# Performance work log

Measured on AMD Instinct MI355X. Metric: run time of the kernel, lower is better.

The kernel has to match this reference:

```python
import jax, jax.numpy as jnp
import numpy as np

B, N, E = 2, 5000, 160000
F_IN, HID, ED = 128, 128, 16
IN_EDGE = 2 * F_IN + 16 + ED  # source, target, radial(4*4), edge_attr


def _lin(k, fan_in, fan_out):
    return (jax.random.normal(k, (fan_in, fan_out), jnp.float32) / np.sqrt(fan_in)).astype(jnp.float32)


def setup_inputs() -> dict:
    key = jax.random.key(0)
    ks = jax.random.split(key, 16)
    h = jax.random.normal(ks[0], (B, N, F_IN), jnp.float32)
    coord = jax.random.normal(ks[1], (B, N, 4, 3), jnp.float32)
    edge_index = jax.random.randint(ks[2], (2, E), 0, N)
    edge_attr = jax.random.normal(ks[3], (E, ED), jnp.float32)
    return {
        "h": h, "coord": coord, "edge_index": edge_index, "edge_attr": edge_attr,
        # edge_mlp: Linear(IN_EDGE->HID), ReLU, Linear(HID->HID), ReLU
        "W_e1": _lin(ks[4], IN_EDGE, HID), "b_e1": jnp.zeros((HID,), jnp.float32),
        "W_e2": _lin(ks[5], HID, HID), "b_e2": jnp.zeros((HID,), jnp.float32),
        # node_mlp: Linear(HID+F_IN->HID), ReLU, Linear(HID->F_IN)
        "W_n1": _lin(ks[6], HID + F_IN, HID), "b_n1": jnp.zeros((HID,), jnp.float32),
        "W_n2": _lin(ks[7], HID, F_IN), "b_n2": jnp.zeros((F_IN,), jnp.float32),
        # coord_mlp: Linear(HID->HID), ReLU, Linear(HID->4, bias=False, xavier gain 0.001)
        "W_c1": _lin(ks[8], HID, HID), "b_c1": jnp.zeros((HID,), jnp.float32),
        "W_c2": _lin(ks[9], HID, 4) * 0.001,
    }


def reference(h, coord, edge_index, edge_attr,
              W_e1, b_e1, W_e2, b_e2,
              W_n1, b_n1, W_n2, b_n2,
              W_c1, b_c1, W_c2):
    row, col = edge_index[0], edge_index[1]
    coords_weight = 1.0
    n_nodes = h.shape[1]

    def single(h_b, coord_b):
        # coord2radial
        cd = coord_b[row] - coord_b[col]                                  # [E,4,3]
        prod = jnp.einsum('ejt,ekt->ejk', cd, cd).reshape(cd.shape[0], -1)  # [E,16]
        nrm = jnp.linalg.norm(prod, axis=-1, keepdims=True)
        radial = prod / jnp.maximum(nrm, 1e-12)                           # F.normalize
        # edge_model
        x = jnp.concatenate([h_b[row], h_b[col], radial, edge_attr], axis=-1)
        ef = jax.nn.relu(jax.nn.relu(x @ W_e1 + b_e1) @ W_e2 + b_e2)      # [E,HID]
        # coord_model: segment mean of cd * coord_mlp(ef)
        w = jax.nn.relu(ef @ W_c1 + b_c1) @ W_c2                          # [E,4]
        trans = cd * w[:, :, None]                                        # [E,4,3]
        agg_c = jax.ops.segment_sum(trans, row, num_segments=n_nodes)     # [N,4,3]
        cnt = jax.ops.segment_sum(jnp.ones((row.shape[0],), trans.dtype), row,
                                  num_segments=n_nodes)                   # [N]
        coord_new = coord_b + (agg_c / jnp.maximum(cnt, 1.0)[:, None, None]) * coords_weight
        # node_model (recurrent)
        agg_h = jax.ops.segment_sum(ef, row, num_segments=n_nodes)        # [N,HID]
        z = jnp.concatenate([h_b, agg_h], axis=-1)
        h_new = h_b + jax.nn.relu(z @ W_n1 + b_n1) @ W_n2 + b_n2
        return h_new, coord_new

    hs, coords = jax.vmap(single)(h, coord)
    return hs, coords
```

## Files before the change

kernel.cpp:

```cpp
#include <hip/hip_runtime.h>
#include <hip/hip_bf16.h>

#define B   2
#define NN_ 5000
#define NE_ 160000
#define F   128
#define HID 128
#define ED  16

typedef __bf16 bf16x8 __attribute__((ext_vector_type(8)));
typedef __bf16 bf16x4 __attribute__((ext_vector_type(4)));
typedef float  f32x4  __attribute__((ext_vector_type(4)));

#define MS  136
#define PS  40
#define EDG 128

__global__ void pack_weights(const float* __restrict__ We1, const float* __restrict__ We2,
                             const float* __restrict__ Wc1, const float* __restrict__ Wc2,
                             __bf16* __restrict__ pw1, __bf16* __restrict__ pw2,
                             __bf16* __restrict__ pwc1, __bf16* __restrict__ pwc2)
{
    int idx = blockIdx.x * 256 + threadIdx.x;
    const float* W; __bf16* P; int KT, Nr, local;
    if (idx < 36864)      { W = We1; P = pw1;  KT = 9; Nr = 128; local = idx; }
    else if (idx < 53248) { W = We2; P = pw2;  KT = 4; Nr = 128; local = idx - 36864; }
    else if (idx < 69632) { W = Wc1; P = pwc1; KT = 4; Nr = 128; local = idx - 53248; }
    else                  { W = Wc2; P = pwc2; KT = 4; Nr = 4;   local = idx - 69632; }
    int j = local & 7, lane = (local >> 3) & 63, rest = local >> 9;
    int kt = rest % KT, nt = rest / KT;
    int k = kt * 32 + (lane >> 4) * 8 + j;
    int n = nt * 16 + (lane & 15);
    float v = (n < Nr) ? W[k * Nr + n] : 0.f;
    P[local] = (__bf16)v;
}

__global__ void hist_kernel(const int* __restrict__ ei, int* __restrict__ csr_cnt)
{
    int i = blockIdx.x * 256 + threadIdx.x;
    if (i < NE_) atomicAdd(&csr_cnt[ei[i]], 1);
}

__global__ void scan_kernel(const int* __restrict__ csr_cnt,
                            int* __restrict__ csr_off, int* __restrict__ csr_pos)
{
    __shared__ int part[256];
    const int t = threadIdx.x;
    int sum = 0;
    #pragma unroll
    for (int j = 0; j < 20; j++) {
        int idx = t * 20 + j;
        if (idx < NN_) sum += csr_cnt[idx];
    }
    part[t] = sum;
    __syncthreads();
    if (t == 0) {
        int run = 0;
        for (int i = 0; i < 256; i++) { int v = part[i]; part[i] = run; run += v; }
    }
    __syncthreads();
    int run = part[t];
    #pragma unroll
    for (int j = 0; j < 20; j++) {
        int idx = t * 20 + j;
        if (idx < NN_) { csr_off[idx] = run; csr_pos[idx] = run; run += csr_cnt[idx]; }
    }
    if (t == 0) csr_off[NN_] = NE_;
}

__global__ void bucket_kernel(const int* __restrict__ ei,
                              int* __restrict__ csr_pos, int* __restrict__ bucket)
{
    int i = blockIdx.x * 256 + threadIdx.x;
    if (i < NE_) { int p = atomicAdd(&csr_pos[ei[i]], 1); bucket[p] = i; }
}

__global__ void ea_sort_kernel(const float* __restrict__ ea, const int* __restrict__ bucket,
                               __bf16* __restrict__ eas)
{
    int idx = blockIdx.x * 256 + threadIdx.x;
    if (idx < NE_ * 4) {
        int p = idx >> 2, j = idx & 3;
        int e = bucket[p];
        float4 v = ((const float4*)ea)[e * 4 + j];
        bf16x4 bv = {(__bf16)v.x, (__bf16)v.y, (__bf16)v.z, (__bf16)v.w};
        *(bf16x4*)&eas[p * 16 + j * 4] = bv;
    }
}

__global__ __launch_bounds__(512) void pre_kernel(
    const float* __restrict__ h, const __bf16* __restrict__ pw1,
    __bf16* __restrict__ pr, __bf16* __restrict__ pc)
{
    __shared__ __align__(16) __bf16 hs[128 * MS];
    const int t = threadIdx.x;
    const int b = blockIdx.y;
    const int n0 = blockIdx.x * 128;
    const int lane = t & 63, wave = t >> 6;
    const int quad = lane >> 4, c = lane & 15;

    #pragma unroll
    for (int it = 0; it < 8; it++) {
        int idx = it * 512 + t;
        int node = idx >> 5, ch = idx & 31;
        int gn = n0 + node;
        float4 v = (gn < NN_) ? *(const float4*)&h[((size_t)b * NN_ + gn) * F + ch * 4]
                              : (float4){0.f, 0.f, 0.f, 0.f};
        bf16x4 bv = {(__bf16)v.x, (__bf16)v.y, (__bf16)v.z, (__bf16)v.w};
        *(bf16x4*)&hs[node * MS + ch * 4] = bv;
    }
    __syncthreads();

    const bf16x8* pw1v = (const bf16x8*)pw1;
    f32x4 accr[8], accc[8];
    #pragma unroll
    for (int m = 0; m < 8; m++) { accr[m] = (f32x4){0,0,0,0}; accc[m] = (f32x4){0,0,0,0}; }
    for (int kt = 0; kt < 4; kt++) {
        bf16x8 wr = pw1v[(wave * 9 + kt) * 64 + lane];
        bf16x8 wc = pw1v[(wave * 9 + kt + 4) * 64 + lane];
        #pragma unroll
        for (int m = 0; m < 8; m++) {
            bf16x8 x = *(const bf16x8*)&hs[(m * 16 + c) * MS + kt * 32 + quad * 8];
            accr[m] = __builtin_amdgcn_mfma_f32_16x16x32_bf16(wr, x, accr[m], 0, 0, 0);
            accc[m] = __builtin_amdgcn_mfma_f32_16x16x32_bf16(wc, x, accc[m], 0, 0, 0);
        }
    }
    #pragma unroll
    for (int m = 0; m < 8; m++) {
        int gn = n0 + m * 16 + c;
        if (gn < NN_) {
            size_t base = ((size_t)b * NN_ + gn) * F + wave * 16 + quad * 4;
            bf16x4 orr = {(__bf16)accr[m][0], (__bf16)accr[m][1], (__bf16)accr[m][2], (__bf16)accr[m][3]};
            bf16x4 occ = {(__bf16)accc[m][0], (__bf16)accc[m][1], (__bf16)accc[m][2], (__bf16)accc[m][3]};
            *(bf16x4*)&pr[base] = orr;
            *(bf16x4*)&pc[base] = occ;
        }
    }
}

__global__ __launch_bounds__(512, 4) void edge_kernel(
    const __bf16* __restrict__ pr, const __bf16* __restrict__ pc,
    const float* __restrict__ coord,
    const int* __restrict__ ei, const __bf16* __restrict__ eas,
    const int* __restrict__ bucket,
    const float* __restrict__ be1, const float* __restrict__ be2,
    const float* __restrict__ bc1,
    const __bf16* __restrict__ pw1, const __bf16* __restrict__ pw2,
    const __bf16* __restrict__ pwc1, const __bf16* __restrict__ pwc2,
    float* __restrict__ agg_h, float* __restrict__ agg_c)
{
    __shared__ __align__(16) __bf16 buf1[EDG * MS];
    __shared__ __align__(16) __bf16 buf2[EDG * MS];
    __shared__ __bf16 cds[EDG][12];
    __shared__ int rs[EDG], cs[EDG];

    const int t = threadIdx.x;
    const int b = blockIdx.y;
    const int p0 = blockIdx.x * EDG;
    const int lane = t & 63, wave = t >> 6;
    const int quad = lane >> 4, c = lane & 15;
    const int mh = wave >> 2, np = wave & 3;

    if (t < EDG) {
        int eid = bucket[p0 + t];
        rs[t] = ei[eid]; cs[t] = ei[NE_ + eid];
    }
    __syncthreads();

    const __bf16* prb = pr + (size_t)b * NN_ * F;
    const __bf16* pcb = pc + (size_t)b * NN_ * F;
    #pragma unroll
    for (int it = 0; it < 4; it++) {
        int idx = it * 512 + t;
        int e = idx >> 4, ch = idx & 15;
        bf16x8 a = *(const bf16x8*)(prb + (size_t)rs[e] * F + ch * 8);
        bf16x8 v = *(const bf16x8*)(pcb + (size_t)cs[e] * F + ch * 8);
        bf16x8 o;
        #pragma unroll
        for (int j = 0; j < 8; j++) o[j] = (__bf16)((float)a[j] + (float)v[j]);
        *(bf16x8*)&buf1[e * MS + ch * 8] = o;
    }
    if (t < EDG) {
        int e = t;
        const float* cr = coord + ((size_t)b * NN_ + rs[e]) * 12;
        const float* cc = coord + ((size_t)b * NN_ + cs[e]) * 12;
        float cd[12];
        #pragma unroll
        for (int j = 0; j < 12; j++) { cd[j] = cr[j] - cc[j]; cds[e][j] = (__bf16)cd[j]; }
        float prod[16]; float ss = 0.f;
        #pragma unroll
        for (int j = 0; j < 4; j++)
            #pragma unroll
            for (int k = 0; k < 4; k++) {
                float p = cd[j*3]*cd[k*3] + cd[j*3+1]*cd[k*3+1] + cd[j*3+2]*cd[k*3+2];
                prod[j*4 + k] = p; ss += p * p;
            }
        float inv = 1.0f / fmaxf(sqrtf(ss), 1e-12f);
        #pragma unroll
        for (int j = 0; j < 16; j++) buf2[e * PS + j] = (__bf16)(prod[j] * inv);
        const uint4* ep = (const uint4*)(eas + (size_t)(p0 + e) * 16);
        *(uint4*)&buf2[e * PS + 16] = ep[0];
        *(uint4*)&buf2[e * PS + 24] = ep[1];
    }
    __syncthreads();

    const bf16x8* pw1v  = (const bf16x8*)pw1;
    const bf16x8* pw2v  = (const bf16x8*)pw2;
    const bf16x8* pwc1v = (const bf16x8*)pwc1;
    const bf16x8* pwc2v = (const bf16x8*)pwc2;

    f32x4 acc1[4][2];
    #pragma unroll
    for (int m = 0; m < 4; m++)
        #pragma unroll
        for (int n = 0; n < 2; n++) acc1[m][n] = (f32x4){0,0,0,0};
    {
        bf16x8 x1[4];
        #pragma unroll
        for (int m = 0; m < 4; m++)
            x1[m] = *(const bf16x8*)&buf2[((mh*4 + m)*16 + c) * PS + quad*8];
        #pragma unroll
        for (int n = 0; n < 2; n++) {
            bf16x8 w = pw1v[((2*np + n)*9 + 8)*64 + lane];
            #pragma unroll
            for (int m = 0; m < 4; m++)
                acc1[m][n] = __builtin_amdgcn_mfma_f32_16x16x32_bf16(w, x1[m], acc1[m][n], 0, 0, 0);
        }
    }
    #pragma unroll
    for (int n = 0; n < 2; n++) {
        int nt = 2*np + n;
        float4 bb = *(const float4*)&be1[nt*16 + quad*4];
        #pragma unroll
        for (int m = 0; m < 4; m++) {
            int row = (mh*4 + m)*16 + c;
            bf16x4 p = *(const bf16x4*)&buf1[row * MS + nt*16 + quad*4];
            bf16x4 o = { (__bf16)fmaxf(acc1[m][n][0] + (float)p[0] + bb.x, 0.f),
                         (__bf16)fmaxf(acc1[m][n][1] + (float)p[1] + bb.y, 0.f),
                         (__bf16)fmaxf(acc1[m][n][2] + (float)p[2] + bb.z, 0.f),
                         (__bf16)fmaxf(acc1[m][n][3] + (float)p[3] + bb.w, 0.f) };
            *(bf16x4*)&buf1[row * MS + nt*16 + quad*4] = o;
        }
    }
    __syncthreads();

    f32x4 acc2[4][2];
    #pragma unroll
    for (int m = 0; m < 4; m++)
        #pragma unroll
        for (int n = 0; n < 2; n++) acc2[m][n] = (f32x4){0,0,0,0};
    for (int kt = 0; kt < 4; kt++) {
        bf16x8 x[4];
        #pragma unroll
        for (int m = 0; m < 4; m++)
            x[m] = *(const bf16x8*)&buf1[((mh*4 + m)*16 + c) * MS + kt*32 + quad*8];
        #pragma unroll
        for (int n = 0; n < 2; n++) {
            bf16x8 w = pw2v[((2*np + n)*4 + kt)*64 + lane];
            #pragma unroll
            for (int m = 0; m < 4; m++)
                acc2[m][n] = __builtin_amdgcn_mfma_f32_16x16x32_bf16(w, x[m], acc2[m][n], 0, 0, 0);
        }
    }
    #pragma unroll
    for (int n = 0; n < 2; n++) {
        int nt = 2*np + n;
        float4 bb = *(const float4*)&be2[nt*16 + quad*4];
        #pragma unroll
        for (int m = 0; m < 4; m++) {
            int row = (mh*4 + m)*16 + c;
            bf16x4 o = { (__bf16)fmaxf(acc2[m][n][0] + bb.x, 0.f),
                         (__bf16)fmaxf(acc2[m][n][1] + bb.y, 0.f),
                         (__bf16)fmaxf(acc2[m][n][2] + bb.z, 0.f),
                         (__bf16)fmaxf(acc2[m][n][3] + bb.w, 0.f) };
            *(bf16x4*)&buf2[row * MS + nt*16 + quad*4] = o;
        }
    }
    __syncthreads();

    f32x4 acc3[4][2];
    #pragma unroll
    for (int m = 0; m < 4; m++)
        #pragma unroll
        for (int n = 0; n < 2; n++) acc3[m][n] = (f32x4){0,0,0,0};
    for (int kt = 0; kt < 4; kt++) {
        bf16x8 x[4];
        #pragma unroll
        for (int m = 0; m < 4; m++)
            x[m] = *(const bf16x8*)&buf2[((mh*4 + m)*16 + c) * MS + kt*32 + quad*8];
        #pragma unroll
        for (int n = 0; n < 2; n++) {
            bf16x8 w = pwc1v[((2*np + n)*4 + kt)*64 + lane];
            #pragma unroll
            for (int m = 0; m < 4; m++)
                acc3[m][n] = __builtin_amdgcn_mfma_f32_16x16x32_bf16(w, x[m], acc3[m][n], 0, 0, 0);
        }
    }
    #pragma unroll
    for (int n = 0; n < 2; n++) {
        int nt = 2*np + n;
        float4 bb = *(const float4*)&bc1[nt*16 + quad*4];
        #pragma unroll
        for (int m = 0; m < 4; m++) {
            int row = (mh*4 + m)*16 + c;
            bf16x4 o = { (__bf16)fmaxf(acc3[m][n][0] + bb.x, 0.f),
                         (__bf16)fmaxf(acc3[m][n][1] + bb.y, 0.f),
                         (__bf16)fmaxf(acc3[m][n][2] + bb.z, 0.f),
                         (__bf16)fmaxf(acc3[m][n][3] + bb.w, 0.f) };
            *(bf16x4*)&buf1[row * MS + nt*16 + quad*4] = o;
        }
    }
    __syncthreads();

    f32x4 accw = (f32x4){0,0,0,0};
    for (int kt = 0; kt < 4; kt++) {
        bf16x8 x = *(const bf16x8*)&buf1[(wave*16 + c) * MS + kt*32 + quad*8];
        accw = __builtin_amdgcn_mfma_f32_16x16x32_bf16(pwc2v[kt*64 + lane], x, accw, 0, 0, 0);
    }
    if (quad == 0) {
        int e = wave*16 + c;
        #pragma unroll
        for (int j = 0; j < 12; j++)
            cds[e][j] = (__bf16)((float)cds[e][j] * accw[j/3]);
    }
    __syncthreads();

    {
        float* aggh_b = agg_h + (size_t)b * NN_ * HID;
        const int col = t & 127, seg = t >> 7;
        float run = 0.f;
        int cur = rs[seg * 32];
        for (int e = seg * 32; e < seg * 32 + 32; e++) {
            int r = rs[e];
            float v = (float)buf2[e * MS + col];
            if (r != cur) {
                atomicAdd(&aggh_b[(size_t)cur * HID + col], run);
                run = 0.f; cur = r;
            }
            run += v;
        }
        atomicAdd(&aggh_b[(size_t)cur * HID + col], run);
    }
    if (t < 96) {
        float* aggc_b = agg_c + (size_t)b * NN_ * 12;
        const int j = t % 12, q = t / 12;
        float run = 0.f;
        int cur = rs[q * 16];
        for (int e = q * 16; e < q * 16 + 16; e++) {
            int r = rs[e];
            float v = (float)cds[e][j];
            if (r != cur) {
                atomicAdd(&aggc_b[(size_t)cur * 12 + j], run);
                run = 0.f; cur = r;
            }
            run += v;
        }
        atomicAdd(&aggc_b[(size_t)cur * 12 + j], run);
    }
}

#define NPB 8
__global__ __launch_bounds__(128) void node_kernel(
    const float* __restrict__ h, const float* __restrict__ agg_h,
    const float* __restrict__ Wn1, const float* __restrict__ bn1,
    const float* __restrict__ Wn2, const float* __restrict__ bn2,
    float* __restrict__ out_h)
{
    __shared__ float zs[NPB][2 * F];
    __shared__ float h1[NPB][HID];
    const int t  = threadIdx.x;
    const int b  = blockIdx.y;
    const int n0 = blockIdx.x * NPB;

    #pragma unroll
    for (int i = 0; i < NPB; i++) {
        size_t base = ((size_t)b * NN_ + n0 + i);
        zs[i][t]     = h[base * F + t];
        zs[i][F + t] = agg_h[base * HID + t];
    }
    __syncthreads();

    float acc[NPB];
    #pragma unroll
    for (int i = 0; i < NPB; i++) acc[i] = bn1[t];
    for (int k = 0; k < 2 * F; k += 4) {
        float w0 = Wn1[(k+0)*HID + t], w1 = Wn1[(k+1)*HID + t];
        float w2 = Wn1[(k+2)*HID + t], w3 = Wn1[(k+3)*HID + t];
        #pragma unroll
        for (int i = 0; i < NPB; i++) {
            float4 xv = *(const float4*)&zs[i][k];
            acc[i] += xv.x*w0 + xv.y*w1 + xv.z*w2 + xv.w*w3;
        }
    }
    __syncthreads();
    #pragma unroll
    for (int i = 0; i < NPB; i++) h1[i][t] = fmaxf(acc[i], 0.f);
    __syncthreads();

    #pragma unroll
    for (int i = 0; i < NPB; i++) acc[i] = bn2[t];
    for (int k = 0; k < HID; k += 4) {
        float w0 = Wn2[(k+0)*F + t], w1 = Wn2[(k+1)*F + t];
        float w2 = Wn2[(k+2)*F + t], w3 = Wn2[(k+3)*F + t];
        #pragma unroll
        for (int i = 0; i < NPB; i++) {
            float4 xv = *(const float4*)&h1[i][k];
            acc[i] += xv.x*w0 + xv.y*w1 + xv.z*w2 + xv.w*w3;
        }
    }
    #pragma unroll
    for (int i = 0; i < NPB; i++) {
        size_t base = ((size_t)b * NN_ + n0 + i);
        out_h[base * F + t] = zs[i][t] + acc[i];
    }
}

__global__ void coord_kernel(
    const float* __restrict__ coord, const float* __restrict__ agg_c,
    const int* __restrict__ csr_off, float* __restrict__ out_c)
{
    int i = blockIdx.x * 256 + threadIdx.x;
    if (i < B * NN_ * 12) {
        int node = i / 12;
        int n = node % NN_;
        float deg = (float)(csr_off[n + 1] - csr_off[n]);
        out_c[i] = coord[i] + agg_c[i] / fmaxf(deg, 1.0f);
    }
}

extern "C" void kernel_launch(void* const* d_in, const int* in_sizes, int n_in,
                              void* d_out, int out_size, void* d_ws, size_t ws_size,
                              hipStream_t stream) {
    const float* h     = (const float*)d_in[0];
    const float* coord = (const float*)d_in[1];
    const int*   ei    = (const int*)d_in[2];
    const float* ea    = (const float*)d_in[3];
    const float* We1   = (const float*)d_in[4];
    const float* be1   = (const float*)d_in[5];
    const float* We2   = (const float*)d_in[6];
    const float* be2   = (const float*)d_in[7];
    const float* Wn1   = (const float*)d_in[8];
    const float* bn1   = (const float*)d_in[9];
    const float* Wn2   = (const float*)d_in[10];
    const float* bn2   = (const float*)d_in[11];
    const float* Wc1   = (const float*)d_in[12];
    const float* bc1   = (const float*)d_in[13];
    const float* Wc2   = (const float*)d_in[14];

    float* out_h = (float*)d_out;
    float* out_c = out_h + (size_t)B * NN_ * F;

    unsigned char* base = (unsigned char*)d_ws;
    __bf16* pw1  = (__bf16*)base;
    __bf16* pw2  = pw1 + 36864;
    __bf16* pwc1 = pw2 + 16384;
    __bf16* pwc2 = pwc1 + 16384;
    unsigned char* dyn = base + 143360;

    int* csr_cnt = (int*)(dyn);
    int* csr_off = (int*)(dyn + 20000);
    int* csr_pos = (int*)(dyn + 40016);
    int* bucket  = (int*)(dyn + 60016);
    float* agg_h = (float*)(dyn + 700016);
    float* agg_c = agg_h + (size_t)B * NN_ * HID;
    __bf16* pr   = (__bf16*)(agg_c + (size_t)B * NN_ * 12);
    __bf16* pc   = pr + (size_t)B * NN_ * F;
    __bf16* eas  = pc + (size_t)B * NN_ * F;

    pack_weights<<<280, 256, 0, stream>>>(We1, We2, Wc1, Wc2, pw1, pw2, pwc1, pwc2);

    hipMemsetAsync(csr_cnt, 0, 20000, stream);
    hipMemsetAsync(agg_h, 0, (size_t)B * NN_ * (HID + 12) * sizeof(float), stream);

    hist_kernel<<<625, 256, 0, stream>>>(ei, csr_cnt);
    scan_kernel<<<1, 256, 0, stream>>>(csr_cnt, csr_off, csr_pos);
    bucket_kernel<<<625, 256, 0, stream>>>(ei, csr_pos, bucket);

    dim3 pg((NN_ + 127) / 128, B);
    pre_kernel<<<pg, 512, 0, stream>>>(h, pw1, pr, pc);

    ea_sort_kernel<<<2500, 256, 0, stream>>>(ea, bucket, eas);

    dim3 eg(NE_ / EDG, B);
    edge_kernel<<<eg, 512, 0, stream>>>(pr, pc, coord, ei, eas, bucket, be1, be2, bc1,
                                        pw1, pw2, pwc1, pwc2, agg_h, agg_c);

    dim3 ng(NN_ / NPB, B);
    node_kernel<<<ng, 128, 0, stream>>>(h, agg_h, Wn1, bn1, Wn2, bn2, out_h);

    int cn = (B * NN_ * 12 + 255) / 256;
    coord_kernel<<<cn, 256, 0, stream>>>(coord, agg_c, csr_off, out_c);
}
```

Measured before the change: 236.6 us.

## Move node MLP to bf16 MFMA, fuse coord update and edge-attr sorting

Rewrites the node MLP from scalar fp32 FMAs into bf16 MFMA tiles, 32 nodes per block, with Wn1/Wn2 prepacked by pack_weights. The coordinate update is folded into the node kernel and the edge-attribute sort into the bucket kernel, which removes two launches. This cuts per-node ALU work and launch overhead. In exchange the node MLP inputs and hidden activations are rounded to bf16, adding precision error.

New measurement: 208.5 us. 11.9% less time.

```diff
diff --git a/kernel.cpp b/kernel.cpp
--- a/kernel.cpp
+++ b/kernel.cpp
@@ -15,18 +15,25 @@
 #define MS  136
 #define PS  40
 #define EDG 128
+#define ZS  264
+#define HS  136
+#define NPB2 32
 
 __global__ void pack_weights(const float* __restrict__ We1, const float* __restrict__ We2,
                              const float* __restrict__ Wc1, const float* __restrict__ Wc2,
+                             const float* __restrict__ Wn1, const float* __restrict__ Wn2,
                              __bf16* __restrict__ pw1, __bf16* __restrict__ pw2,
-                             __bf16* __restrict__ pwc1, __bf16* __restrict__ pwc2)
+                             __bf16* __restrict__ pwc1, __bf16* __restrict__ pwc2,
+                             __bf16* __restrict__ pwn1, __bf16* __restrict__ pwn2)
 {
     int idx = blockIdx.x * 256 + threadIdx.x;
     const float* W; __bf16* P; int KT, Nr, local;
-    if (idx < 36864)      { W = We1; P = pw1;  KT = 9; Nr = 128; local = idx; }
-    else if (idx < 53248) { W = We2; P = pw2;  KT = 4; Nr = 128; local = idx - 36864; }
-    else if (idx < 69632) { W = Wc1; P = pwc1; KT = 4; Nr = 128; local = idx - 53248; }
-    else                  { W = Wc2; P = pwc2; KT = 4; Nr = 4;   local = idx - 69632; }
+    if (idx < 36864)       { W = We1; P = pw1;  KT = 9; Nr = 128; local = idx; }
+    else if (idx < 53248)  { W = We2; P = pw2;  KT = 4; Nr = 128; local = idx - 36864; }
+    else if (idx < 69632)  { W = Wc1; P = pwc1; KT = 4; Nr = 128; local = idx - 53248; }
+    else if (idx < 71680)  { W = Wc2; P = pwc2; KT = 4; Nr = 4;   local = idx - 69632; }
+    else if (idx < 104448) { W = Wn1; P = pwn1; KT = 8; Nr = 128; local = idx - 71680; }
+    else                   { W = Wn2; P = pwn2; KT = 4; Nr = 128; local = idx - 104448; }
     int j = local & 7, lane = (local >> 3) & 63, rest = local >> 9;
     int kt = rest % KT, nt = rest / KT;
     int k = kt * 32 + (lane >> 4) * 8 + j;
@@ -68,23 +75,22 @@
     if (t == 0) csr_off[NN_] = NE_;
 }
 
-__global__ void bucket_kernel(const int* __restrict__ ei,
-                              int* __restrict__ csr_pos, int* __restrict__ bucket)
+__global__ void bucket_kernel(const int* __restrict__ ei, const float* __restrict__ ea,
+                              int* __restrict__ csr_pos, int* __restrict__ bucket,
+                              __bf16* __restrict__ eas)
 {
     int i = blockIdx.x * 256 + threadIdx.x;
-    if (i < NE_) { int p = atomicAdd(&csr_pos[ei[i]], 1); bucket[p] = i; }
-}
-
-__global__ void ea_sort_kernel(const float* __restrict__ ea, const int* __restrict__ bucket,
-                               __bf16* __restrict__ eas)
-{
-    int idx = blockIdx.x * 256 + threadIdx.x;
-    if (idx < NE_ * 4) {
-        int p = idx >> 2, j = idx & 3;
-        int e = bucket[p];
-        float4 v = ((const float4*)ea)[e * 4 + j];
-        bf16x4 bv = {(__bf16)v.x, (__bf16)v.y, (__bf16)v.z, (__bf16)v.w};
-        *(bf16x4*)&eas[p * 16 + j * 4] = bv;
+    if (i < NE_) {
+        int p = atomicAdd(&csr_pos[ei[i]], 1);
+        bucket[p] = i;
+        const float4* src = (const float4*)(ea + (size_t)i * ED);
+        __bf16* dst = eas + (size_t)p * ED;
+        #pragma unroll
+        for (int j = 0; j < 4; j++) {
+            float4 v = src[j];
+            bf16x4 bv = {(__bf16)v.x, (__bf16)v.y, (__bf16)v.z, (__bf16)v.w};
+            *(bf16x4*)&dst[j * 4] = bv;
+        }
     }
 }
 
@@ -359,72 +365,127 @@
     }
 }
 
-#define NPB 8
-__global__ __launch_bounds__(128) void node_kernel(
+__global__ __launch_bounds__(256) void node_kernel(
     const float* __restrict__ h, const float* __restrict__ agg_h,
-    const float* __restrict__ Wn1, const float* __restrict__ bn1,
-    const float* __restrict__ Wn2, const float* __restrict__ bn2,
-    float* __restrict__ out_h)
-{
-    __shared__ float zs[NPB][2 * F];
-    __shared__ float h1[NPB][HID];
-    const int t  = threadIdx.x;
-    const int b  = blockIdx.y;
-    const int n0 = blockIdx.x * NPB;
-
-    #pragma unroll
-    for (int i = 0; i < NPB; i++) {
-        size_t base = ((size_t)b * NN_ + n0 + i);
-        zs[i][t]     = h[base * F + t];
-        zs[i][F + t] = agg_h[base * HID + t];
-    }
-    __syncthreads();
-
-    float acc[NPB];
-    #pragma unroll
-    for (int i = 0; i < NPB; i++) acc[i] = bn1[t];
-    for (int k = 0; k < 2 * F; k += 4) {
-        float w0 = Wn1[(k+0)*HID + t], w1 = Wn1[(k+1)*HID + t];
-        float w2 = Wn1[(k+2)*HID + t], w3 = Wn1[(k+3)*HID + t];
-        #pragma unroll
-        for (int i = 0; i < NPB; i++) {
-            float4 xv = *(const float4*)&zs[i][k];
-            acc[i] += xv.x*w0 + xv.y*w1 + xv.z*w2 + xv.w*w3;
-        }
-    }
-    __syncthreads();
-    #pragma unroll
-    for (int i = 0; i < NPB; i++) h1[i][t] = fmaxf(acc[i], 0.f);
-    __syncthreads();
-
-    #pragma unroll
-    for (int i = 0; i < NPB; i++) acc[i] = bn2[t];
-    for (int k = 0; k < HID; k += 4) {
-        float w0 = Wn2[(k+0)*F + t], w1 = Wn2[(k+1)*F + t];
-        float w2 = Wn2[(k+2)*F + t], w3 = Wn2[(k+3)*F + t];
-        #pragma unroll
-        for (int i = 0; i < NPB; i++) {
-            float4 xv = *(const float4*)&h1[i][k];
-            acc[i] += xv.x*w0 + xv.y*w1 + xv.z*w2 + xv.w*w3;
-        }
-    }
-    #pragma unroll
-    for (int i = 0; i < NPB; i++) {
-        size_t base = ((size_t)b * NN_ + n0 + i);
-        out_h[base * F + t] = zs[i][t] + acc[i];
-    }
-}
-
-__global__ void coord_kernel(
-    const float* __restrict__ coord, const float* __restrict__ agg_c,
-    const int* __restrict__ csr_off, float* __restrict__ out_c)
-{
-    int i = blockIdx.x * 256 + threadIdx.x;
-    if (i < B * NN_ * 12) {
-        int node = i / 12;
-        int n = node % NN_;
-        float deg = (float)(csr_off[n + 1] - csr_off[n]);
-        out_c[i] = coord[i] + agg_c[i] / fmaxf(deg, 1.0f);
+    const float* __restrict__ agg_c, const float* __restrict__ coord,
+    const int* __restrict__ csr_off,
+    const __bf16* __restrict__ pwn1, const float* __restrict__ bn1,
+    const __bf16* __restrict__ pwn2, const float* __restrict__ bn2,
+    float* __restrict__ out_h, float* __restrict__ out_c)
+{
+    __shared__ __align__(16) __bf16 zs[NPB2 * ZS];
+    __shared__ __align__(16) __bf16 h1s[NPB2 * HS];
+    const int t = threadIdx.x;
+    const int b = blockIdx.y;
+    const int n0 = blockIdx.x * NPB2;
+    const int lane = t & 63, wave = t >> 6;
+    const int quad = lane >> 4, c = lane & 15;
+
+    #pragma unroll
+    for (int it = 0; it < 8; it++) {
+        int idx = it * 256 + t;
+        int node = idx >> 6, ch = idx & 63;
+        int gn = n0 + node;
+        float4 v = (float4){0.f, 0.f, 0.f, 0.f};
+        if (gn < NN_) {
+            const float* src = (ch < 32) ? &h[((size_t)b * NN_ + gn) * F + ch * 4]
+                                         : &agg_h[((size_t)b * NN_ + gn) * HID + (ch - 32) * 4];
+            v = *(const float4*)src;
+        }
+        bf16x4 bv = {(__bf16)v.x, (__bf16)v.y, (__bf16)v.z, (__bf16)v.w};
+        *(bf16x4*)&zs[node * ZS + ch * 4] = bv;
+    }
+    __syncthreads();
+
+    const bf16x8* w1v = (const bf16x8*)pwn1;
+    const bf16x8* w2v = (const bf16x8*)pwn2;
+    f32x4 a1[2][2];
+    #pragma unroll
+    for (int m = 0; m < 2; m++)
+        #pragma unroll
+        for (int n = 0; n < 2; n++) a1[m][n] = (f32x4){0,0,0,0};
+    for (int kt = 0; kt < 8; kt++) {
+        bf16x8 x[2];
+        #pragma unroll
+        for (int m = 0; m < 2; m++)
+            x[m] = *(const bf16x8*)&zs[(m*16 + c) * ZS + kt*32 + quad*8];
+        #pragma unroll
+        for (int n = 0; n < 2; n++) {
+            bf16x8 w = w1v[((2*wave + n)*8 + kt)*64 + lane];
+            #pragma unroll
+            for (int m = 0; m < 2; m++)
+                a1[m][n] = __builtin_amdgcn_mfma_f32_16x16x32_bf16(w, x[m], a1[m][n], 0, 0, 0);
+        }
+    }
+    __syncthreads();
+    #pragma unroll
+    for (int n = 0; n < 2; n++) {
+        int nt = 2*wave + n;
+        float4 bb = *(const float4*)&bn1[nt*16 + quad*4];
+        #pragma unroll
+        for (int m = 0; m < 2; m++) {
+            bf16x4 o = { (__bf16)fmaxf(a1[m][n][0] + bb.x, 0.f),
+                         (__bf16)fmaxf(a1[m][n][1] + bb.y, 0.f),
+                         (__bf16)fmaxf(a1[m][n][2] + bb.z, 0.f),
+                         (__bf16)fmaxf(a1[m][n][3] + bb.w, 0.f) };
+            *(bf16x4*)&h1s[(m*16 + c) * HS + nt*16 + quad*4] = o;
+        }
+    }
+    __syncthreads();
+
+    f32x4 a2[2][2];
+    #pragma unroll
+    for (int m = 0; m < 2; m++)
+        #pragma unroll
+        for (int n = 0; n < 2; n++) a2[m][n] = (f32x4){0,0,0,0};
+    for (int kt = 0; kt < 4; kt++) {
+        bf16x8 x[2];
+        #pragma unroll
+        for (int m = 0; m < 2; m++)
+            x[m] = *(const bf16x8*)&h1s[(m*16 + c) * HS + kt*32 + quad*8];
+        #pragma unroll
+        for (int n = 0; n < 2; n++) {
+            bf16x8 w = w2v[((2*wave + n)*4 + kt)*64 + lane];
+            #pragma unroll
+            for (int m = 0; m < 2; m++)
+                a2[m][n] = __builtin_amdgcn_mfma_f32_16x16x32_bf16(w, x[m], a2[m][n], 0, 0, 0);
+        }
+    }
+    float* os = (float*)zs;
+    #pragma unroll
+    for (int n = 0; n < 2; n++) {
+        int nt = 2*wave + n;
+        float4 bb = *(const float4*)&bn2[nt*16 + quad*4];
+        #pragma unroll
+        for (int m = 0; m < 2; m++) {
+            f32x4 o = { a2[m][n][0] + bb.x, a2[m][n][1] + bb.y,
+                        a2[m][n][2] + bb.z, a2[m][n][3] + bb.w };
+            *(f32x4*)&os[(m*16 + c) * 132 + nt*16 + quad*4] = o;
+        }
+    }
+    __syncthreads();
+
+    #pragma unroll
+    for (int it = 0; it < 4; it++) {
+        int idx = it * 256 + t;
+        int node = idx >> 5, ch = idx & 31;
+        int gn = n0 + node;
+        if (gn < NN_) {
+            size_t gb = ((size_t)b * NN_ + gn) * F + ch * 4;
+            float4 hres = *(const float4*)&h[gb];
+            float4 acc = *(const float4*)&os[node * 132 + ch * 4];
+            float4 o = { hres.x + acc.x, hres.y + acc.y, hres.z + acc.z, hres.w + acc.w };
+            *(float4*)&out_h[gb] = o;
+        }
+    }
+    for (int idx = t; idx < NPB2 * 12; idx += 256) {
+        int node = idx / 12, j = idx % 12;
+        int gn = n0 + node;
+        if (gn < NN_) {
+            float deg = (float)(csr_off[gn + 1] - csr_off[gn]);
+            size_t ci = ((size_t)b * NN_ + gn) * 12 + j;
+            out_c[ci] = coord[ci] + agg_c[ci] / fmaxf(deg, 1.0f);
+        }
     }
 }
 
@@ -455,7 +516,9 @@
     __bf16* pw2  = pw1 + 36864;
     __bf16* pwc1 = pw2 + 16384;
     __bf16* pwc2 = pwc1 + 16384;
-    unsigned char* dyn = base + 143360;
+    __bf16* pwn1 = pwc2 + 2048;
+    __bf16* pwn2 = pwn1 + 32768;
+    unsigned char* dyn = base + 241664;
 
     int* csr_cnt = (int*)(dyn);
     int* csr_off = (int*)(dyn + 20000);
@@ -467,27 +530,24 @@
     __bf16* pc   = pr + (size_t)B * NN_ * F;
     __bf16* eas  = pc + (size_t)B * NN_ * F;
 
-    pack_weights<<<280, 256, 0, stream>>>(We1, We2, Wc1, Wc2, pw1, pw2, pwc1, pwc2);
+    pack_weights<<<472, 256, 0, stream>>>(We1, We2, Wc1, Wc2, Wn1, Wn2,
+                                          pw1, pw2, pwc1, pwc2, pwn1, pwn2);
 
     hipMemsetAsync(csr_cnt, 0, 20000, stream);
     hipMemsetAsync(agg_h, 0, (size_t)B * NN_ * (HID + 12) * sizeof(float), stream);
 
     hist_kernel<<<625, 256, 0, stream>>>(ei, csr_cnt);
     scan_kernel<<<1, 256, 0, stream>>>(csr_cnt, csr_off, csr_pos);
-    bucket_kernel<<<625, 256, 0, stream>>>(ei, csr_pos, bucket);
+    bucket_kernel<<<625, 256, 0, stream>>>(ei, ea, csr_pos, bucket, eas);
 
     dim3 pg((NN_ + 127) / 128, B);
     pre_kernel<<<pg, 512, 0, stream>>>(h, pw1, pr, pc);
-
-    ea_sort_kernel<<<2500, 256, 0, stream>>>(ea, bucket, eas);
 
     dim3 eg(NE_ / EDG, B);
     edge_kernel<<<eg, 512, 0, stream>>>(pr, pc, coord, ei, eas, bucket, be1, be2, bc1,
                                         pw1, pw2, pwc1, pwc2, agg_h, agg_c);
 
-    dim3 ng(NN_ / NPB, B);
-    node_kernel<<<ng, 128, 0, stream>>>(h, agg_h, Wn1, bn1, Wn2, bn2, out_h);
-
-    int cn = (B * NN_ * 12 + 255) / 256;
-    coord_kernel<<<cn, 256, 0, stream>>>(coord, agg_c, csr_off, out_c);
-}
+    dim3 ng((NN_ + NPB2 - 1) / NPB2, B);
+    node_kernel<<<ng, 256, 0, stream>>>(h, agg_h, agg_c, coord, csr_off,
+                                        pwn1, bn1, pwn2, bn2, out_h, out_c);
+}
```
